# Performance work log

Measured on AMD Instinct MI355X. Metric: run time of the kernel, lower is better.

Reference implementation:

```python
import jax, jax.numpy as jnp
import numpy as np
import math

L = 500
B = 4
E = 100_000
NBINS = 24  # periodic cubic spline intervals between 25 knots


def setup_inputs() -> dict:
    key = jax.random.key(0)
    k1, k2, k3, k4, k5, k6 = jax.random.split(key, 6)
    N = jax.random.normal(k1, (B, L, 3), dtype=jnp.float32) * 3.0
    CA = jax.random.normal(k2, (B, L, 3), dtype=jnp.float32) * 3.0
    CB = jax.random.normal(k3, (B, L, 3), dtype=jnp.float32) * 3.0
    coeff = jax.random.normal(k4, (L, L, NBINS, 4), dtype=jnp.float32) * 0.1
    x_idx = jax.random.randint(k5, (E,), 0, L, dtype=jnp.int32)
    off = jax.random.randint(k6, (E,), 1, L, dtype=jnp.int32)
    y_idx = ((x_idx + off) % L).astype(jnp.int32)  # guarantees i != j (off-diagonal mask)
    return {"N": N, "CA": CA, "CB": CB, "coeff": coeff, "x_idx": x_idx, "y_idx": y_idx}


def _cross(a, b):
    return jnp.cross(a, b)


def reference(N, CA, CB, coeff, x_idx, y_idx):
    # gather atom coords per edge: [B, E, 3]
    xN = N[:, x_idx]
    xCA = CA[:, x_idx]
    xCB = CB[:, x_idx]
    yCB = CB[:, y_idx]

    # dihedral (N_i, CA_i, CB_i, CB_j)
    b1 = xCA - xN
    b2 = xCB - xCA
    b3 = yCB - xCB
    n1 = _cross(b1, b2)
    n2 = _cross(b2, b3)
    b2u = b2 / jnp.linalg.norm(b2, axis=-1, keepdims=True)
    m = _cross(n1, b2u)
    theta = jnp.arctan2(jnp.sum(m * n2, -1), jnp.sum(n1 * n2, -1))  # [B, E]

    # periodic cubic spline evaluation over 25 knots
    step = 15.0 * math.pi / 180.0
    cutoffs = jnp.linspace(-math.pi + 0.5 * step, math.pi + 0.5 * step, 25).astype(theta.dtype)
    two_pi = jnp.asarray(2.0 * math.pi, theta.dtype)
    theta_w = jnp.where(theta < cutoffs[0], theta + two_pi, theta)  # wrap into knot range
    seg = jnp.clip(jnp.searchsorted(cutoffs, theta_w, side='right') - 1, 0, NBINS - 1)  # [B, E]

    c_pair = coeff[x_idx, y_idx]                    # [E, NBINS, 4]
    csel = c_pair[jnp.arange(E)[None, :], seg]      # [B, E, 4]
    t = theta_w - cutoffs[seg]
    # Horner: c0 + c1*t + c2*t^2 + c3*t^3
    val = ((csel[..., 3] * t + csel[..., 2]) * t + csel[..., 1]) * t + csel[..., 0]
    return jnp.sum(val)
```

## Files before the change

kernel.cpp:

```cpp
#include <hip/hip_runtime.h>
#include <math.h>

#define LL 500
#define BB 4
#define EE 100000
#define NBINS 24
#define TOTAL (BB * EE)
#define BLOCK 256
#define NB1 512
#define COORD_F (BB * LL * 3)

struct f3 { float x, y, z; };

__device__ __forceinline__ f3 ld3(const float* __restrict__ p) {
    f3 r; r.x = p[0]; r.y = p[1]; r.z = p[2]; return r;
}
__device__ __forceinline__ f3 sub3(f3 a, f3 b) {
    f3 r; r.x = a.x - b.x; r.y = a.y - b.y; r.z = a.z - b.z; return r;
}
__device__ __forceinline__ f3 cross3(f3 a, f3 b) {
    f3 r;
    r.x = a.y * b.z - a.z * b.y;
    r.y = a.z * b.x - a.x * b.z;
    r.z = a.x * b.y - a.y * b.x;
    return r;
}
__device__ __forceinline__ float dot3(f3 a, f3 b) {
    return fmaf(a.x, b.x, fmaf(a.y, b.y, a.z * b.z));
}

__global__ void __launch_bounds__(BLOCK) theta_partial_kernel(
    const float* __restrict__ N,
    const float* __restrict__ CA,
    const float* __restrict__ CB,
    const float* __restrict__ coeff,
    const int* __restrict__ x_idx,
    const int* __restrict__ y_idx,
    float* __restrict__ partials)
{
    __shared__ float lds[3 * COORD_F];
    {
        const float4* s0 = reinterpret_cast<const float4*>(N);
        const float4* s1 = reinterpret_cast<const float4*>(CA);
        const float4* s2 = reinterpret_cast<const float4*>(CB);
        float4* d0 = reinterpret_cast<float4*>(&lds[0]);
        float4* d1 = reinterpret_cast<float4*>(&lds[COORD_F]);
        float4* d2 = reinterpret_cast<float4*>(&lds[2 * COORD_F]);
        for (int j = threadIdx.x; j < COORD_F / 4; j += BLOCK) {
            d0[j] = s0[j];
            d1[j] = s1[j];
            d2[j] = s2[j];
        }
    }
    __syncthreads();

    const float step  = 0.261799387799149436f;
    const float c0    = -3.14159265358979324f + 0.5f * step;
    const float twoPi = 6.28318530717958648f;

    float acc = 0.0f;
    for (int i = blockIdx.x * BLOCK + threadIdx.x; i < TOTAL; i += NB1 * BLOCK) {
        const int e = i >> 2;
        const int b = i & 3;
        const int x = x_idx[e];
        const int y = y_idx[e];

        const float* Nb  = &lds[b * (LL * 3)];
        const float* CAb = &lds[COORD_F + b * (LL * 3)];
        const float* CBb = &lds[2 * COORD_F + b * (LL * 3)];

        const f3 xN  = ld3(Nb  + 3 * x);
        const f3 xCA = ld3(CAb + 3 * x);
        const f3 xCB = ld3(CBb + 3 * x);
        const f3 yCB = ld3(CBb + 3 * y);

        const f3 b1 = sub3(xCA, xN);
        const f3 b2 = sub3(xCB, xCA);
        const f3 b3 = sub3(yCB, xCB);

        const f3 n1 = cross3(b1, b2);
        const f3 n2 = cross3(b2, b3);

        const float rn = rsqrtf(dot3(b2, b2));
        const f3 m = cross3(n1, b2);
        const float s = dot3(m, n2) * rn;
        const float c = dot3(n1, n2);

        const float theta = atan2f(s, c);

        const float tw = (theta < c0) ? theta + twoPi : theta;

        int seg = (int)floorf((tw - c0) / step);
        seg = seg < 0 ? 0 : (seg > NBINS - 1 ? NBINS - 1 : seg);

        const float t = tw - (c0 + (float)seg * step);

        const float4 cs = *reinterpret_cast<const float4*>(
            coeff + (((size_t)x * LL + (size_t)y) * NBINS + (size_t)seg) * 4);

        acc += fmaf(fmaf(fmaf(cs.w, t, cs.z), t, cs.y), t, cs.x);
    }

    #pragma unroll
    for (int off = 32; off > 0; off >>= 1)
        acc += __shfl_down(acc, off, 64);

    __shared__ float wsum[BLOCK / 64];
    const int lane = threadIdx.x & 63;
    const int wid  = threadIdx.x >> 6;
    if (lane == 0) wsum[wid] = acc;
    __syncthreads();
    if (threadIdx.x == 0)
        partials[blockIdx.x] = wsum[0] + wsum[1] + wsum[2] + wsum[3];
}

__global__ void __launch_bounds__(BLOCK) theta_reduce_kernel(
    const float* __restrict__ partials,
    float* __restrict__ out)
{
    float v = partials[threadIdx.x] + partials[threadIdx.x + BLOCK];

    #pragma unroll
    for (int off = 32; off > 0; off >>= 1)
        v += __shfl_down(v, off, 64);

    __shared__ float wsum[BLOCK / 64];
    const int lane = threadIdx.x & 63;
    const int wid  = threadIdx.x >> 6;
    if (lane == 0) wsum[wid] = v;
    __syncthreads();
    if (threadIdx.x == 0)
        out[0] = wsum[0] + wsum[1] + wsum[2] + wsum[3];
}

extern "C" void kernel_launch(void* const* d_in, const int* in_sizes, int n_in,
                              void* d_out, int out_size, void* d_ws, size_t ws_size,
                              hipStream_t stream) {
    const float* N     = (const float*)d_in[0];
    const float* CA    = (const float*)d_in[1];
    const float* CB    = (const float*)d_in[2];
    const float* coeff = (const float*)d_in[3];
    const int* x_idx   = (const int*)d_in[4];
    const int* y_idx   = (const int*)d_in[5];
    float* out      = (float*)d_out;
    float* partials = (float*)d_ws;

    theta_partial_kernel<<<NB1, BLOCK, 0, stream>>>(N, CA, CB, coeff,
                                                    x_idx, y_idx, partials);
    theta_reduce_kernel<<<1, BLOCK, 0, stream>>>(partials, out);
}
```

Baseline: 14.04 us.

## Split work per batch so each block stages only one batch's coordinates

Each block now handles a single batch and a fixed chunk of 512 edges, so it loads only that batch's N/CA/CB coordinates (18 KB) into LDS instead of all four batches (72 KB). The grid grows from 512 to 784 blocks and the grid-stride loop becomes two fixed items per thread. The smaller LDS footprint lets more blocks be resident per CU and cuts the redundant staging traffic. In exchange, adjacent threads no longer share an edge across batches, so the coefficient gathers lose that locality, and the reduce kernel loops over more partials.

```diff
diff --git a/kernel.cpp b/kernel.cpp
--- a/kernel.cpp
+++ b/kernel.cpp
@@ -5,16 +5,14 @@
 #define BB 4
 #define EE 100000
 #define NBINS 24
-#define TOTAL (BB * EE)
 #define BLOCK 256
-#define NB1 512
-#define COORD_F (BB * LL * 3)
+#define CHUNK 512
+#define NCHUNK ((EE + CHUNK - 1) / CHUNK)
+#define GRID1 (BB * NCHUNK)
+#define CF (LL * 3)
 
 struct f3 { float x, y, z; };
 
-__device__ __forceinline__ f3 ld3(const float* __restrict__ p) {
-    f3 r; r.x = p[0]; r.y = p[1]; r.z = p[2]; return r;
-}
 __device__ __forceinline__ f3 sub3(f3 a, f3 b) {
     f3 r; r.x = a.x - b.x; r.y = a.y - b.y; r.z = a.z - b.z; return r;
 }
@@ -29,6 +27,48 @@
     return fmaf(a.x, b.x, fmaf(a.y, b.y, a.z * b.z));
 }
 
+__device__ __forceinline__ float item_val(
+    const float* __restrict__ lN, const float* __restrict__ lCA,
+    const float* __restrict__ lCB, const float* __restrict__ coeff,
+    int x, int y)
+{
+    f3 xN, xCA, xCB, yCB;
+    xN.x  = lN [3 * x];     xN.y  = lN [3 * x + 1]; xN.z  = lN [3 * x + 2];
+    xCA.x = lCA[3 * x];     xCA.y = lCA[3 * x + 1]; xCA.z = lCA[3 * x + 2];
+    xCB.x = lCB[3 * x];     xCB.y = lCB[3 * x + 1]; xCB.z = lCB[3 * x + 2];
+    yCB.x = lCB[3 * y];     yCB.y = lCB[3 * y + 1]; yCB.z = lCB[3 * y + 2];
+
+    const f3 b1 = sub3(xCA, xN);
+    const f3 b2 = sub3(xCB, xCA);
+    const f3 b3 = sub3(yCB, xCB);
+
+    const f3 n1 = cross3(b1, b2);
+    const f3 n2 = cross3(b2, b3);
+
+    const float rn = rsqrtf(dot3(b2, b2));
+    const f3 m = cross3(n1, b2);
+    const float s = dot3(m, n2) * rn;
+    const float c = dot3(n1, n2);
+
+    const float theta = atan2f(s, c);
+
+    const float step  = 0.261799387799149436f;
+    const float c0    = -3.14159265358979324f + 0.5f * step;
+    const float twoPi = 6.28318530717958648f;
+
+    const float tw = (theta < c0) ? theta + twoPi : theta;
+
+    int seg = (int)floorf((tw - c0) / step);
+    seg = seg < 0 ? 0 : (seg > NBINS - 1 ? NBINS - 1 : seg);
+
+    const float t = tw - (c0 + (float)seg * step);
+
+    const float4 cs = *reinterpret_cast<const float4*>(
+        coeff + (((size_t)x * LL + (size_t)y) * NBINS + (size_t)seg) * 4);
+
+    return fmaf(fmaf(fmaf(cs.w, t, cs.z), t, cs.y), t, cs.x);
+}
+
 __global__ void __launch_bounds__(BLOCK) theta_partial_kernel(
     const float* __restrict__ N,
     const float* __restrict__ CA,
@@ -38,15 +78,18 @@
     const int* __restrict__ y_idx,
     float* __restrict__ partials)
 {
-    __shared__ float lds[3 * COORD_F];
+    const int b     = blockIdx.x & 3;
+    const int chunk = blockIdx.x >> 2;
+
+    __shared__ float lds[3 * CF];
     {
-        const float4* s0 = reinterpret_cast<const float4*>(N);
-        const float4* s1 = reinterpret_cast<const float4*>(CA);
-        const float4* s2 = reinterpret_cast<const float4*>(CB);
+        const float4* s0 = reinterpret_cast<const float4*>(N  + b * CF);
+        const float4* s1 = reinterpret_cast<const float4*>(CA + b * CF);
+        const float4* s2 = reinterpret_cast<const float4*>(CB + b * CF);
         float4* d0 = reinterpret_cast<float4*>(&lds[0]);
-        float4* d1 = reinterpret_cast<float4*>(&lds[COORD_F]);
-        float4* d2 = reinterpret_cast<float4*>(&lds[2 * COORD_F]);
-        for (int j = threadIdx.x; j < COORD_F / 4; j += BLOCK) {
+        float4* d1 = reinterpret_cast<float4*>(&lds[CF]);
+        float4* d2 = reinterpret_cast<float4*>(&lds[2 * CF]);
+        for (int j = threadIdx.x; j < CF / 4; j += BLOCK) {
             d0[j] = s0[j];
             d1[j] = s1[j];
             d2[j] = s2[j];
@@ -54,51 +97,21 @@
     }
     __syncthreads();
 
-    const float step  = 0.261799387799149436f;
-    const float c0    = -3.14159265358979324f + 0.5f * step;
-    const float twoPi = 6.28318530717958648f;
+    const float* lN  = &lds[0];
+    const float* lCA = &lds[CF];
+    const float* lCB = &lds[2 * CF];
+
+    const int e0 = chunk * CHUNK + threadIdx.x;
+    const int e1 = e0 + BLOCK;
 
     float acc = 0.0f;
-    for (int i = blockIdx.x * BLOCK + threadIdx.x; i < TOTAL; i += NB1 * BLOCK) {
-        const int e = i >> 2;
-        const int b = i & 3;
-        const int x = x_idx[e];
-        const int y = y_idx[e];
-
-        const float* Nb  = &lds[b * (LL * 3)];
-        const float* CAb = &lds[COORD_F + b * (LL * 3)];
-        const float* CBb = &lds[2 * COORD_F + b * (LL * 3)];
-
-        const f3 xN  = ld3(Nb  + 3 * x);
-        const f3 xCA = ld3(CAb + 3 * x);
-        const f3 xCB = ld3(CBb + 3 * x);
-        const f3 yCB = ld3(CBb + 3 * y);
-
-        const f3 b1 = sub3(xCA, xN);
-        const f3 b2 = sub3(xCB, xCA);
-        const f3 b3 = sub3(yCB, xCB);
-
-        const f3 n1 = cross3(b1, b2);
-        const f3 n2 = cross3(b2, b3);
-
-        const float rn = rsqrtf(dot3(b2, b2));
-        const f3 m = cross3(n1, b2);
-        const float s = dot3(m, n2) * rn;
-        const float c = dot3(n1, n2);
-
-        const float theta = atan2f(s, c);
-
-        const float tw = (theta < c0) ? theta + twoPi : theta;
-
-        int seg = (int)floorf((tw - c0) / step);
-        seg = seg < 0 ? 0 : (seg > NBINS - 1 ? NBINS - 1 : seg);
-
-        const float t = tw - (c0 + (float)seg * step);
-
-        const float4 cs = *reinterpret_cast<const float4*>(
-            coeff + (((size_t)x * LL + (size_t)y) * NBINS + (size_t)seg) * 4);
-
-        acc += fmaf(fmaf(fmaf(cs.w, t, cs.z), t, cs.y), t, cs.x);
+    if (e0 < EE) {
+        const int x0 = x_idx[e0], y0 = y_idx[e0];
+        acc += item_val(lN, lCA, lCB, coeff, x0, y0);
+    }
+    if (e1 < EE) {
+        const int x1 = x_idx[e1], y1 = y_idx[e1];
+        acc += item_val(lN, lCA, lCB, coeff, x1, y1);
     }
 
     #pragma unroll
@@ -118,7 +131,9 @@
     const float* __restrict__ partials,
     float* __restrict__ out)
 {
-    float v = partials[threadIdx.x] + partials[threadIdx.x + BLOCK];
+    float v = 0.0f;
+    for (int i = threadIdx.x; i < GRID1; i += BLOCK)
+        v += partials[i];
 
     #pragma unroll
     for (int off = 32; off > 0; off >>= 1)
@@ -145,7 +160,7 @@
     float* out      = (float*)d_out;
     float* partials = (float*)d_ws;
 
-    theta_partial_kernel<<<NB1, BLOCK, 0, stream>>>(N, CA, CB, coeff,
-                                                    x_idx, y_idx, partials);
+    theta_partial_kernel<<<GRID1, BLOCK, 0, stream>>>(N, CA, CB, coeff,
+                                                      x_idx, y_idx, partials);
     theta_reduce_kernel<<<1, BLOCK, 0, stream>>>(partials, out);
 }
```

Measured after the change: 16.57 us. +18.0%, slower.

## Fuse final reduction via last-block atomic counter and hoist index loads before LDS fill

Applied to the files above, without the earlier changes.

Replaces the two-kernel partial-plus-reduce scheme with one kernel. Each block publishes its partial sum, and the last block to bump an atomic counter performs the final reduction. The grid-stride loop is fully unrolled into a fixed four items per thread, and the x/y index loads are issued before the shared-memory coordinate fill so their latency overlaps it. This saves a second kernel launch and gap, but adds a memset launch for the counter plus atomic traffic.

```diff
diff --git a/kernel.cpp b/kernel.cpp
--- a/kernel.cpp
+++ b/kernel.cpp
@@ -8,13 +8,13 @@
 #define TOTAL (BB * EE)
 #define BLOCK 256
 #define NB1 512
+#define STRIDE (NB1 * BLOCK)
 #define COORD_F (BB * LL * 3)
+
+#define PART_OFF 32
 
 struct f3 { float x, y, z; };
 
-__device__ __forceinline__ f3 ld3(const float* __restrict__ p) {
-    f3 r; r.x = p[0]; r.y = p[1]; r.z = p[2]; return r;
-}
 __device__ __forceinline__ f3 sub3(f3 a, f3 b) {
     f3 r; r.x = a.x - b.x; r.y = a.y - b.y; r.z = a.z - b.z; return r;
 }
@@ -29,15 +29,76 @@
     return fmaf(a.x, b.x, fmaf(a.y, b.y, a.z * b.z));
 }
 
-__global__ void __launch_bounds__(BLOCK) theta_partial_kernel(
+__device__ __forceinline__ float item_val(
+    const float* __restrict__ lds, const float* __restrict__ coeff,
+    int b, int x, int y)
+{
+    const float* lN  = &lds[b * (LL * 3)];
+    const float* lCA = &lds[COORD_F + b * (LL * 3)];
+    const float* lCB = &lds[2 * COORD_F + b * (LL * 3)];
+
+    f3 xN, xCA, xCB, yCB;
+    xN.x  = lN [3 * x]; xN.y  = lN [3 * x + 1]; xN.z  = lN [3 * x + 2];
+    xCA.x = lCA[3 * x]; xCA.y = lCA[3 * x + 1]; xCA.z = lCA[3 * x + 2];
+    xCB.x = lCB[3 * x]; xCB.y = lCB[3 * x + 1]; xCB.z = lCB[3 * x + 2];
+    yCB.x = lCB[3 * y]; yCB.y = lCB[3 * y + 1]; yCB.z = lCB[3 * y + 2];
+
+    const f3 b1 = sub3(xCA, xN);
+    const f3 b2 = sub3(xCB, xCA);
+    const f3 b3 = sub3(yCB, xCB);
+
+    const f3 n1 = cross3(b1, b2);
+    const f3 n2 = cross3(b2, b3);
+
+    const float rn = rsqrtf(dot3(b2, b2));
+    const f3 m = cross3(n1, b2);
+    const float s = dot3(m, n2) * rn;
+    const float c = dot3(n1, n2);
+
+    const float theta = atan2f(s, c);
+
+    const float step  = 0.261799387799149436f;
+    const float c0    = -3.14159265358979324f + 0.5f * step;
+    const float twoPi = 6.28318530717958648f;
+
+    const float tw = (theta < c0) ? theta + twoPi : theta;
+
+    int seg = (int)floorf((tw - c0) / step);
+    seg = seg < 0 ? 0 : (seg > NBINS - 1 ? NBINS - 1 : seg);
+
+    const float t = tw - (c0 + (float)seg * step);
+
+    const float4 cs = *reinterpret_cast<const float4*>(
+        coeff + (((size_t)x * LL + (size_t)y) * NBINS + (size_t)seg) * 4);
+
+    return fmaf(fmaf(fmaf(cs.w, t, cs.z), t, cs.y), t, cs.x);
+}
+
+__global__ void __launch_bounds__(BLOCK) theta_fused_kernel(
     const float* __restrict__ N,
     const float* __restrict__ CA,
     const float* __restrict__ CB,
     const float* __restrict__ coeff,
     const int* __restrict__ x_idx,
     const int* __restrict__ y_idx,
-    float* __restrict__ partials)
+    unsigned int* __restrict__ counter,
+    float* __restrict__ partials,
+    float* __restrict__ out)
 {
+    const int base = blockIdx.x * BLOCK + threadIdx.x;
+    const int b    = base & 3;
+    const int e0   = base >> 2;
+
+    const bool has3 = (base + 3 * STRIDE) < TOTAL;
+    const int x0 = x_idx[e0];
+    const int y0 = y_idx[e0];
+    const int x1 = x_idx[e0 + STRIDE / 4];
+    const int y1 = y_idx[e0 + STRIDE / 4];
+    const int x2 = x_idx[e0 + 2 * (STRIDE / 4)];
+    const int y2 = y_idx[e0 + 2 * (STRIDE / 4)];
+    const int x3 = has3 ? x_idx[e0 + 3 * (STRIDE / 4)] : 0;
+    const int y3 = has3 ? y_idx[e0 + 3 * (STRIDE / 4)] : 0;
+
     __shared__ float lds[3 * COORD_F];
     {
         const float4* s0 = reinterpret_cast<const float4*>(N);
@@ -54,83 +115,47 @@
     }
     __syncthreads();
 
-    const float step  = 0.261799387799149436f;
-    const float c0    = -3.14159265358979324f + 0.5f * step;
-    const float twoPi = 6.28318530717958648f;
-
-    float acc = 0.0f;
-    for (int i = blockIdx.x * BLOCK + threadIdx.x; i < TOTAL; i += NB1 * BLOCK) {
-        const int e = i >> 2;
-        const int b = i & 3;
-        const int x = x_idx[e];
-        const int y = y_idx[e];
-
-        const float* Nb  = &lds[b * (LL * 3)];
-        const float* CAb = &lds[COORD_F + b * (LL * 3)];
-        const float* CBb = &lds[2 * COORD_F + b * (LL * 3)];
-
-        const f3 xN  = ld3(Nb  + 3 * x);
-        const f3 xCA = ld3(CAb + 3 * x);
-        const f3 xCB = ld3(CBb + 3 * x);
-        const f3 yCB = ld3(CBb + 3 * y);
-
-        const f3 b1 = sub3(xCA, xN);
-        const f3 b2 = sub3(xCB, xCA);
-        const f3 b3 = sub3(yCB, xCB);
-
-        const f3 n1 = cross3(b1, b2);
-        const f3 n2 = cross3(b2, b3);
-
-        const float rn = rsqrtf(dot3(b2, b2));
-        const f3 m = cross3(n1, b2);
-        const float s = dot3(m, n2) * rn;
-        const float c = dot3(n1, n2);
-
-        const float theta = atan2f(s, c);
-
-        const float tw = (theta < c0) ? theta + twoPi : theta;
-
-        int seg = (int)floorf((tw - c0) / step);
-        seg = seg < 0 ? 0 : (seg > NBINS - 1 ? NBINS - 1 : seg);
-
-        const float t = tw - (c0 + (float)seg * step);
-
-        const float4 cs = *reinterpret_cast<const float4*>(
-            coeff + (((size_t)x * LL + (size_t)y) * NBINS + (size_t)seg) * 4);
-
-        acc += fmaf(fmaf(fmaf(cs.w, t, cs.z), t, cs.y), t, cs.x);
-    }
+    float acc = item_val(lds, coeff, b, x0, y0)
+              + item_val(lds, coeff, b, x1, y1)
+              + item_val(lds, coeff, b, x2, y2);
+    if (has3) acc += item_val(lds, coeff, b, x3, y3);
 
     #pragma unroll
     for (int off = 32; off > 0; off >>= 1)
         acc += __shfl_down(acc, off, 64);
 
     __shared__ float wsum[BLOCK / 64];
+    __shared__ int is_last;
     const int lane = threadIdx.x & 63;
     const int wid  = threadIdx.x >> 6;
     if (lane == 0) wsum[wid] = acc;
     __syncthreads();
-    if (threadIdx.x == 0)
-        partials[blockIdx.x] = wsum[0] + wsum[1] + wsum[2] + wsum[3];
-}
 
-__global__ void __launch_bounds__(BLOCK) theta_reduce_kernel(
-    const float* __restrict__ partials,
-    float* __restrict__ out)
-{
-    float v = partials[threadIdx.x] + partials[threadIdx.x + BLOCK];
+    if (threadIdx.x == 0) {
+        const float p = wsum[0] + wsum[1] + wsum[2] + wsum[3];
+        __hip_atomic_store(&partials[blockIdx.x], p,
+                           __ATOMIC_RELEASE, __HIP_MEMORY_SCOPE_AGENT);
+        const unsigned int old = __hip_atomic_fetch_add(
+            counter, 1u, __ATOMIC_ACQ_REL, __HIP_MEMORY_SCOPE_AGENT);
+        is_last = (old == NB1 - 1) ? 1 : 0;
+    }
+    __syncthreads();
 
-    #pragma unroll
-    for (int off = 32; off > 0; off >>= 1)
-        v += __shfl_down(v, off, 64);
+    if (is_last) {
+        float v = __hip_atomic_load(&partials[threadIdx.x],
+                                    __ATOMIC_ACQUIRE, __HIP_MEMORY_SCOPE_AGENT)
+                + __hip_atomic_load(&partials[threadIdx.x + BLOCK],
+                                    __ATOMIC_ACQUIRE, __HIP_MEMORY_SCOPE_AGENT);
+        #pragma unroll
+        for (int off = 32; off > 0; off >>= 1)
+            v += __shfl_down(v, off, 64);
 
-    __shared__ float wsum[BLOCK / 64];
-    const int lane = threadIdx.x & 63;
-    const int wid  = threadIdx.x >> 6;
-    if (lane == 0) wsum[wid] = v;
-    __syncthreads();
-    if (threadIdx.x == 0)
-        out[0] = wsum[0] + wsum[1] + wsum[2] + wsum[3];
+        __shared__ float wsum2[BLOCK / 64];
+        if (lane == 0) wsum2[wid] = v;
+        __syncthreads();
+        if (threadIdx.x == 0)
+            out[0] = wsum2[0] + wsum2[1] + wsum2[2] + wsum2[3];
+    }
 }
 
 extern "C" void kernel_launch(void* const* d_in, const int* in_sizes, int n_in,
@@ -142,10 +167,14 @@
     const float* coeff = (const float*)d_in[3];
     const int* x_idx   = (const int*)d_in[4];
     const int* y_idx   = (const int*)d_in[5];
-    float* out      = (float*)d_out;
-    float* partials = (float*)d_ws;
+    float* out = (float*)d_out;
 
-    theta_partial_kernel<<<NB1, BLOCK, 0, stream>>>(N, CA, CB, coeff,
-                                                    x_idx, y_idx, partials);
-    theta_reduce_kernel<<<1, BLOCK, 0, stream>>>(partials, out);
+    unsigned int* counter = (unsigned int*)d_ws;
+    float* partials = (float*)d_ws + PART_OFF;
+
+    hipMemsetAsync(counter, 0, sizeof(unsigned int), stream);
+
+    theta_fused_kernel<<<NB1, BLOCK, 0, stream>>>(N, CA, CB, coeff,
+                                                  x_idx, y_idx,
+                                                  counter, partials, out);
 }
```

After: 32.79 us. 133% more time.
